# Performance work log

Measured on AMD Instinct MI355X. Metric: run time of the kernel, lower is better.

## Reference

```python
import jax, jax.numpy as jnp
import numpy as np

B, S, D, H, L, K = 16, 384, 512, 8, 4, 7
HD = D // H
MAXLEN = 400


def _pos_encoding(d=D, max_len=MAXLEN):
    # Faithful to the (unusual) torch loop: even idx i -> sin(pos/10000**(2i/d)),
    # odd idx i+1 -> cos(pos/10000**(2(i+1)/d))
    pe = np.zeros((max_len, d), dtype=np.float32)
    pos = np.arange(max_len, dtype=np.float64)[:, None]
    i = np.arange(0, d, 2)
    pe[:, i] = np.sin(pos / 10000.0 ** (2 * i / d))
    pe[:, i + 1] = np.cos(pos / 10000.0 ** (2 * (i + 1) / d))
    return jnp.asarray(pe)

POS_ENC = _pos_encoding()


def layer_norm(x, g, b, eps=1e-5):
    m = jnp.mean(x, -1, keepdims=True)
    v = jnp.mean((x - m) ** 2, -1, keepdims=True)
    return (x - m) * jax.lax.rsqrt(v + eps) * g + b


def dsconv(x, dw_w, pw_w, pw_b):
    # x: [B,S,D]; depthwise conv1d (no bias) then pointwise 1x1 (bias)
    xc = jnp.transpose(x, (0, 2, 1))  # [B,D,S]
    y = jax.lax.conv_general_dilated(
        xc, dw_w, window_strides=(1,), padding=[(K // 2, K // 2)],
        dimension_numbers=("NCH", "OIH", "NCH"), feature_group_count=D)  # [B,D,S]
    return jnp.einsum("bcs,oc->bso", y, pw_w) + pw_b  # [B,S,D]


def setup_inputs():
    key = jax.random.key(0)
    ks = jax.random.split(key, 16)
    sc = 0.02
    inp = {
        "x": jax.random.normal(ks[0], (B, S, D), jnp.float32),
        "mask": jax.random.randint(ks[1], (B, S), 0, 2, jnp.int32),
        "dw_w": jax.random.normal(ks[2], (L, D, 1, K), jnp.float32) * sc,
        "pw_w": jax.random.normal(ks[3], (L, D, D), jnp.float32) * sc,
        "pw_b": jnp.zeros((L, D), jnp.float32),
        "conv_ln_g": jnp.ones((L, D), jnp.float32),
        "conv_ln_b": jnp.zeros((L, D), jnp.float32),
        "pos_ln_g": jnp.ones((D,), jnp.float32),
        "pos_ln_b": jnp.zeros((D,), jnp.float32),
        "wq": jax.random.normal(ks[4], (D, D), jnp.float32) * sc,
        "bq": jnp.zeros((D,), jnp.float32),
        "wk": jax.random.normal(ks[5], (D, D), jnp.float32) * sc,
        "bk": jnp.zeros((D,), jnp.float32),
        "wv": jax.random.normal(ks[6], (D, D), jnp.float32) * sc,
        "bv": jnp.zeros((D,), jnp.float32),
        "wo": jax.random.normal(ks[7], (D, D), jnp.float32) * sc,
        "bo": jnp.zeros((D,), jnp.float32),
        "ff_ln_g": jnp.ones((D,), jnp.float32),
        "ff_ln_b": jnp.zeros((D,), jnp.float32),
        "ff_w": jax.random.normal(ks[8], (D, D), jnp.float32) * sc,
        "ff_b": jnp.zeros((D,), jnp.float32),
    }
    return inp


def attention(x, mask, wq, bq, wk, bk, wv, bv, wo, bo):
    def heads(w, b):
        y = jnp.einsum("bsd,od->bso", x, w) + b
        return jnp.transpose(y.reshape(B, S, H, HD), (0, 2, 1, 3))  # [B,H,S,HD]
    q, k, v = heads(wq, bq), heads(wk, bk), heads(wv, bv)
    energy = jnp.einsum("bhqd,bhkd->bhqk", q, k) / jnp.sqrt(jnp.float32(HD))
    m = (mask == 1)[:, None, None, :]  # [B,1,1,S]
    energy = jnp.where(m, jnp.float32(-1e10), energy)
    alpha = jax.nn.softmax(energy, axis=-1)  # dropout = identity (eval)
    a = jnp.einsum("bhqk,bhkd->bhqd", alpha, v)
    a = jnp.transpose(a, (0, 2, 1, 3)).reshape(B, S, D)
    return jnp.einsum("bsd,od->bso", a, wo) + bo


def reference(x, mask, dw_w, pw_w, pw_b, conv_ln_g, conv_ln_b, pos_ln_g, pos_ln_b,
              wq, bq, wk, bk, wv, bv, wo, bo, ff_ln_g, ff_ln_b, ff_w, ff_b):
    out = x + POS_ENC[None, :S, :]
    res = out
    out = layer_norm(out, pos_ln_g, pos_ln_b)
    for i in range(L):
        out = jax.nn.relu(dsconv(out, dw_w[i], pw_w[i], pw_b[i]))
        out = out + res  # dropout = identity (eval)
        res = out
        out = layer_norm(out, conv_ln_g[i], conv_ln_b[i])
    out = attention(out, mask, wq, bq, wk, bk, wv, bv, wo, bo)
    out = out + res
    res = out
    out = layer_norm(out, ff_ln_g, ff_ln_b)
    out = jax.nn.relu(jnp.einsum("bsd,od->bso", out, ff_w) + ff_b)
    return out + res
```

## Files before the change

kernel.cpp:

```cpp
#include <hip/hip_runtime.h>

#define BB 16
#define SS 384
#define DD 512
#define HH 8
#define HDIM 64
#define LLAY 4
#define KW 7
#define MM (BB*SS)

typedef unsigned short u16;
typedef unsigned int u32;
typedef short short8v __attribute__((ext_vector_type(8)));
typedef float floatx4 __attribute__((ext_vector_type(4)));

__device__ __forceinline__ float bf2f(u16 u) {
    union { u32 i; float f; } v; v.i = ((u32)u) << 16; return v.f;
}
__device__ __forceinline__ u16 f2bf(float f) {
    union { float f; u32 i; } v; v.f = f;
    return (u16)((v.i + 0x7FFFu + ((v.i >> 16) & 1u)) >> 16);
}
__device__ __forceinline__ bool sniff_f32(const void* dtp) {
    return *((const u32*)dtp) == 0x3F800000u;
}
__device__ __forceinline__ float ldf(const void* p, long i, bool f32) {
    return f32 ? ((const float*)p)[i] : bf2f(((const u16*)p)[i]);
}
__device__ __forceinline__ short8v ldfrag_scalar(const void* p, long i, bool f32) {
    short8v r;
    if (f32) {
        const float* q = (const float*)p + i;
#pragma unroll
        for (int j = 0; j < 8; j++) r[j] = (short)f2bf(q[j]);
    } else {
        r = *(const short8v*)((const u16*)p + i);
    }
    return r;
}

__device__ __forceinline__ void load_lds16(const u16* g, u16* l) {
    __builtin_amdgcn_global_load_lds((const __attribute__((address_space(1))) void*)g,
                                     (__attribute__((address_space(3))) void*)l, 16, 0, 0);
}
__device__ __forceinline__ int swz(int row) { return (row & 3) ^ ((row >> 2) & 3); }
__device__ __forceinline__ short8v lds_frag(const u16* buf, int row, int quad) {
    return *(const short8v*)(buf + ((size_t)row * 4 + (quad ^ swz(row))) * 8);
}

__device__ __forceinline__ floatx4 mfma16(short8v a, short8v b, floatx4 c) {
    return __builtin_amdgcn_mfma_f32_16x16x32_bf16(a, b, c, 0, 0, 0);
}

#define WCV_DW 2359296
#define WCV_TOT (WCV_DW + LLAY*KW*DD)
#define NCVB ((WCV_TOT + 255) / 256)

__global__ __launch_bounds__(256) void posln_cvt_kernel(
    const void* __restrict__ x, const void* __restrict__ g, const void* __restrict__ bvec,
    u16* __restrict__ res, u16* __restrict__ out,
    const void* __restrict__ pw_w, const void* __restrict__ wq,
    const void* __restrict__ wk, const void* __restrict__ wv,
    const void* __restrict__ wo, const void* __restrict__ ff_w,
    const void* __restrict__ dw_w, u16* __restrict__ wdst,
    const void* __restrict__ dtp) {
    const bool f32 = sniff_f32(dtp);
    const int tid = threadIdx.x;
    if (blockIdx.x >= MM) {
        const int i = (blockIdx.x - MM) * 256 + tid;
        if (i >= WCV_TOT) return;
        const void* src; long idx;
        if (i < 1048576) { src = pw_w; idx = i; }
        else if (i < WCV_DW) {
            const int j = i - 1048576;
            const int m = j >> 18;
            idx = j & 262143;
            src = (m == 0) ? wq : (m == 1) ? wk : (m == 2) ? wv : (m == 3) ? wo : ff_w;
        } else {
            const int j = i - WCV_DW;
            const int l = j / (KW * DD);
            const int r1 = j % (KW * DD);
            const int t = r1 / DD, c = r1 % DD;
            src = dw_w; idx = ((long)l * DD + c) * KW + t;
        }
        wdst[i] = f2bf(ldf(src, idx, f32));
        return;
    }
    const int row = blockIdx.x;
    const int s = row % SS;
    float v[2];
#pragma unroll
    for (int i = 0; i < 2; i++) {
        const int d = tid + i * 256;
        const float freq = __expf(-(float)d * 0.035977892078032f);
        const float arg = (float)s * freq;
        const float pe = (d & 1) ? __cosf(arg) : __sinf(arg);
        v[i] = ldf(x, (long)row * DD + d, f32) + pe;
        res[row * DD + d] = f2bf(v[i]);
    }
    float sum = v[0] + v[1], sq = v[0] * v[0] + v[1] * v[1];
#pragma unroll
    for (int off = 32; off; off >>= 1) { sum += __shfl_down(sum, off); sq += __shfl_down(sq, off); }
    __shared__ float red[4][2];
    const int wv2 = tid >> 6;
    if ((tid & 63) == 0) { red[wv2][0] = sum; red[wv2][1] = sq; }
    __syncthreads();
    sum = red[0][0] + red[1][0] + red[2][0] + red[3][0];
    sq  = red[0][1] + red[1][1] + red[2][1] + red[3][1];
    const float mean = sum * (1.f / DD);
    const float rstd = rsqrtf(sq * (1.f / DD) - mean * mean + 1e-5f);
#pragma unroll
    for (int i = 0; i < 2; i++) {
        const int d = tid + i * 256;
        out[row * DD + d] = f2bf((v[i] - mean) * rstd * ldf(g, d, f32) + ldf(bvec, d, f32));
    }
}

__global__ __launch_bounds__(512) void lnres_kernel(const u16* __restrict__ y,
                                                    const void* __restrict__ g,
                                                    const void* __restrict__ bvec,
                                                    int blayer,
                                                    u16* __restrict__ out,
                                                    const void* __restrict__ dtp) {
    const bool f32 = sniff_f32(dtp);
    const long voff = (long)blayer * DD;
    const int row = blockIdx.x * 8 + (threadIdx.x >> 6);
    const int lane = threadIdx.x & 63;
    const short8v v = *(const short8v*)(y + (size_t)row * DD + lane * 8);
    float f[8], sum = 0.f, sq = 0.f;
#pragma unroll
    for (int j = 0; j < 8; j++) { f[j] = bf2f((u16)v[j]); sum += f[j]; sq += f[j] * f[j]; }
#pragma unroll
    for (int off = 32; off; off >>= 1) { sum += __shfl_xor(sum, off); sq += __shfl_xor(sq, off); }
    const float mean = sum * (1.f / DD);
    const float rstd = rsqrtf(sq * (1.f / DD) - mean * mean + 1e-5f);
    short8v o;
#pragma unroll
    for (int j = 0; j < 8; j++) {
        const int d = lane * 8 + j;
        o[j] = (short)f2bf((f[j] - mean) * rstd * ldf(g, voff + d, f32) + ldf(bvec, voff + d, f32));
    }
    *(short8v*)(out + (size_t)row * DD + lane * 8) = o;
}

template <int VEC>
__global__ __launch_bounds__(256) void dwconv_kernel(const u16* __restrict__ in,
                                                     const void* __restrict__ w, int layer,
                                                     u16* __restrict__ out,
                                                     const void* __restrict__ dtp) {
    if constexpr (VEC) {
        const int bsw = (blockIdx.x & 7) * (MM * DD / 8 / 256 / 8) + (blockIdx.x >> 3);
        const int idx = bsw * 256 + threadIdx.x;
        const int c8 = (idx & 63) * 8;
        const int ms = idx >> 6;
        const int s = ms % SS;
        const u16* wl = (const u16*)w + (size_t)layer * KW * DD;
        float acc[8] = {0, 0, 0, 0, 0, 0, 0, 0};
#pragma unroll
        for (int t = 0; t < KW; t++) {
            const int ss2 = s + t - 3;
            if (ss2 >= 0 && ss2 < SS) {
                const short8v iv = *(const short8v*)(in + (size_t)(ms + t - 3) * DD + c8);
                const short8v wv = *(const short8v*)(wl + t * DD + c8);
#pragma unroll
                for (int j = 0; j < 8; j++)
                    acc[j] += bf2f((u16)iv[j]) * bf2f((u16)wv[j]);
            }
        }
        short8v ov;
#pragma unroll
        for (int j = 0; j < 8; j++) ov[j] = (short)f2bf(acc[j]);
        *(short8v*)(out + (size_t)ms * DD + c8) = ov;
    } else {
        const bool f32 = sniff_f32(dtp);
        const long woff = (long)layer * DD * KW;
        const int idx = blockIdx.x * 256 + threadIdx.x;
        const int c = idx & (DD - 1);
        const int ms = idx >> 9;
        const int s = ms % SS;
        float acc = 0.f;
#pragma unroll
        for (int t = 0; t < KW; t++) {
            const int ss2 = s + t - 3;
            if (ss2 >= 0 && ss2 < SS)
                acc += bf2f(in[(ms + t - 3) * DD + c]) * ldf(w, woff + c * KW + t, f32);
        }
        out[idx] = f2bf(acc);
    }
}

__device__ __forceinline__ void stage32(const u16* A, const u16* Wp, int m0,
                                        u16* Ab, u16* Wb, int tid, int k0) {
#pragma unroll
    for (int j = 0; j < 2; j++) {
        const int c = j * 256 + tid;
        const int row = c >> 2;
        const int kp = (c & 3) ^ swz(row);
        load_lds16(Wp + (size_t)row * DD + k0 + kp * 8, Wb + (size_t)c * 8);
    }
    if (tid < 128) {
        const int row = tid >> 2;
        const int kp = (tid & 3) ^ swz(row);
        load_lds16(A + (size_t)(m0 + row) * DD + k0 + kp * 8, Ab + (size_t)tid * 8);
    }
}

__device__ __forceinline__ void kloop32(const u16* A, const u16* Wp, int m0,
                                        u16* Abuf, u16* Wbuf,
                                        int tid, int wave, int ln15, int quad,
                                        floatx4 acc[2][2]) {
    stage32(A, Wp, m0, Abuf, Wbuf, tid, 0);
    __syncthreads();
    for (int ks = 0; ks < 16; ks++) {
        const int cur = ks & 1;
        u16* Ab = Abuf + cur * (32 * 32);
        u16* Wb = Wbuf + cur * (128 * 32);
        if (ks < 15)
            stage32(A, Wp, m0, Abuf + (cur ^ 1) * (32 * 32),
                    Wbuf + (cur ^ 1) * (128 * 32), tid, (ks + 1) * 32);
        const short8v a0 = lds_frag(Ab, ln15, quad);
        const short8v a1 = lds_frag(Ab, 16 + ln15, quad);
#pragma unroll
        for (int nt = 0; nt < 2; nt++) {
            const short8v b = lds_frag(Wb, wave * 32 + nt * 16 + ln15, quad);
            acc[0][nt] = mfma16(a0, b, acc[0][nt]);
            acc[1][nt] = mfma16(a1, b, acc[1][nt]);
        }
        __syncthreads();
    }
}

template <int RELU, int FINAL>
__global__ __launch_bounds__(256) void gemm32w_kernel(
    const u16* __restrict__ A, const u16* __restrict__ W,
    const void* __restrict__ bias, int blayer,
    const u16* __restrict__ res_in, u16* __restrict__ res_out,
    void* __restrict__ out, const void* __restrict__ dtp) {
    const bool f32 = sniff_f32(dtp);
    const long voff = (long)blayer * DD;
    __shared__ __align__(16) u16 smem[10240];
    u16* Wbuf = smem;
    u16* Abuf = smem + 8192;
    const int tid = threadIdx.x;
    const int m0 = blockIdx.x * 32, n0 = blockIdx.y * 128;
    const int wave = tid >> 6, lane = tid & 63;
    const int ln15 = lane & 15, quad = lane >> 4;

    floatx4 acc[2][2];
#pragma unroll
    for (int mt = 0; mt < 2; mt++)
#pragma unroll
        for (int nt = 0; nt < 2; nt++) acc[mt][nt] = {0.f, 0.f, 0.f, 0.f};

    kloop32(A, W + (size_t)n0 * DD, m0, Abuf, Wbuf, tid, wave, ln15, quad, acc);

#pragma unroll
    for (int nt = 0; nt < 2; nt++) {
        const int col = n0 + wave * 32 + nt * 16 + ln15;
        const float bval = ldf(bias, voff + col, f32);
#pragma unroll
        for (int mt = 0; mt < 2; mt++)
#pragma unroll
            for (int r = 0; r < 4; r++) {
                const int m = m0 + mt * 16 + quad * 4 + r;
                float y = acc[mt][nt][r] + bval;
                if (RELU) y = fmaxf(y, 0.f);
                y += bf2f(res_in[(size_t)m * DD + col]);
                if (res_out) res_out[(size_t)m * DD + col] = f2bf(y);
                if constexpr (FINAL) {
                    if (f32) ((float*)out)[(size_t)m * DD + col] = y;
                    else     ((u16*)out)[(size_t)m * DD + col] = f2bf(y);
                }
            }
    }
}

__device__ __forceinline__ void stage64(const u16* A, const u16* Wp, int m0,
                                        u16* Ab, u16* Wb, int tid, int k0) {
#pragma unroll
    for (int j = 0; j < 2; j++) {
        const int c = j * 256 + tid;
        const int row = c >> 2;
        const int kp = (c & 3) ^ swz(row);
        load_lds16(Wp + (size_t)row * DD + k0 + kp * 8, Wb + (size_t)c * 8);
    }
    {
        const int row = tid >> 2;
        const int kp = (tid & 3) ^ swz(row);
        load_lds16(A + (size_t)(m0 + row) * DD + k0 + kp * 8, Ab + (size_t)tid * 8);
    }
}

__device__ __forceinline__ void kloop64(const u16* A, const u16* Wp, int m0,
                                        u16* Abuf, u16* Wbuf,
                                        int tid, int wm, int wn, int ln15, int quad,
                                        floatx4 acc[2][4]) {
    stage64(A, Wp, m0, Abuf, Wbuf, tid, 0);
    __syncthreads();
    for (int ks = 0; ks < 16; ks++) {
        const int cur = ks & 1;
        u16* Ab = Abuf + cur * (64 * 32);
        u16* Wb = Wbuf + cur * (128 * 32);
        if (ks < 15)
            stage64(A, Wp, m0, Abuf + (cur ^ 1) * (64 * 32),
                    Wbuf + (cur ^ 1) * (128 * 32), tid, (ks + 1) * 32);
        const short8v a0 = lds_frag(Ab, wm * 32 + ln15, quad);
        const short8v a1 = lds_frag(Ab, wm * 32 + 16 + ln15, quad);
#pragma unroll
        for (int nt = 0; nt < 4; nt++) {
            const short8v b = lds_frag(Wb, wn * 64 + nt * 16 + ln15, quad);
            acc[0][nt] = mfma16(a0, b, acc[0][nt]);
            acc[1][nt] = mfma16(a1, b, acc[1][nt]);
        }
        __syncthreads();
    }
}

#define VP 72
__global__ __launch_bounds__(256, 4) void qkv64_kernel(
    const u16* __restrict__ A,
    const u16* __restrict__ Wq, const u16* __restrict__ Wk, const u16* __restrict__ Wv,
    const void* __restrict__ bq, const void* __restrict__ bk, const void* __restrict__ bv,
    u16* __restrict__ qo, u16* __restrict__ ko, u16* __restrict__ vo,
    const void* __restrict__ dtp) {
    const bool f32 = sniff_f32(dtp);
    const int sel = blockIdx.z;
    const u16* W = (sel == 0) ? Wq : (sel == 1) ? Wk : Wv;
    const void* bias = (sel == 0) ? bq : (sel == 1) ? bk : bv;

    __shared__ __align__(16) u16 smem[12288];
    u16* Wbuf = smem;
    u16* Abuf = smem + 8192;
    u16 (*vtile)[VP] = (u16 (*)[VP])smem;

    const int tid = threadIdx.x;
    const int m0 = blockIdx.x * 64, n0 = blockIdx.y * 128;
    const int wave = tid >> 6, lane = tid & 63;
    const int wm = wave >> 1, wn = wave & 1;
    const int ln15 = lane & 15, quad = lane >> 4;
    const int bidx = m0 / SS;

    floatx4 acc[2][4];
#pragma unroll
    for (int mt = 0; mt < 2; mt++)
#pragma unroll
        for (int nt = 0; nt < 4; nt++) acc[mt][nt] = {0.f, 0.f, 0.f, 0.f};

    kloop64(A, W + (size_t)n0 * DD, m0, Abuf, Wbuf, tid, wm, wn, ln15, quad, acc);

    if (sel == 2) {
#pragma unroll
        for (int nt = 0; nt < 4; nt++) {
            const int cl = wn * 64 + nt * 16 + ln15;
            const float bval = ldf(bias, n0 + cl, f32);
#pragma unroll
            for (int mt = 0; mt < 2; mt++)
#pragma unroll
                for (int r = 0; r < 4; r++)
                    vtile[cl][wm * 32 + mt * 16 + quad * 4 + r] = f2bf(acc[mt][nt][r] + bval);
        }
        __syncthreads();
        const int c = tid & 127, half = tid >> 7;
        const int col = n0 + c;
        const int h = col >> 6, hd = col & 63;
        u16* dst = vo + ((size_t)(bidx * HH + h) * HDIM + hd) * SS
                      + (m0 - bidx * SS) + half * 32;
        const u16* srcl = &vtile[c][half * 32];
#pragma unroll
        for (int j = 0; j < 4; j++)
            *(short8v*)(dst + j * 8) = *(const short8v*)(srcl + j * 8);
    } else {
        u16* out = (sel == 0) ? qo : ko;
#pragma unroll
        for (int nt = 0; nt < 4; nt++) {
            const int col = n0 + wn * 64 + nt * 16 + ln15;
            const int h = col >> 6, hd = col & 63;
            const float bval = ldf(bias, col, f32);
#pragma unroll
            for (int mt = 0; mt < 2; mt++)
#pragma unroll
                for (int r = 0; r < 4; r++) {
                    const int m = m0 + wm * 32 + mt * 16 + quad * 4 + r;
                    const int s = m - bidx * SS;
                    out[((size_t)(bidx * HH + h) * SS + s) * HDIM + hd] = f2bf(acc[mt][nt][r] + bval);
                }
        }
    }
}

template <int RELU, int DO_LN, int FINAL>
__global__ __launch_bounds__(512, 4) void gemm16_kernel(
    const u16* __restrict__ A, const void* __restrict__ W, int wlayer,
    const void* __restrict__ bias, const void* __restrict__ g,
    const void* __restrict__ bvec, int blayer,
    const u16* __restrict__ res_in, u16* __restrict__ res_out,
    void* __restrict__ out, const void* __restrict__ dtp) {
    const bool f32 = sniff_f32(dtp);
    const long woff = (long)wlayer * DD * DD;
    const long voff = (long)blayer * DD;
    __shared__ float part[8][16][2];
    const int tid = threadIdx.x;
    const int m0 = blockIdx.x * 16;
    const int wave = tid >> 6, lane = tid & 63;
    const int ln15 = lane & 15, quad = lane >> 4;

    floatx4 acc[4];
#pragma unroll
    for (int nt = 0; nt < 4; nt++) acc[nt] = {0.f, 0.f, 0.f, 0.f};

    const u16* A0 = A + (size_t)(m0 + ln15) * DD + quad * 8;
#pragma unroll
    for (int ks = 0; ks < 16; ks++) {
        const int k0 = ks * 32;
        short8v a0 = *(const short8v*)(A0 + k0);
        short8v b[4];
#pragma unroll
        for (int nt = 0; nt < 4; nt++) {
            const long wrow = woff + (long)(wave * 64 + nt * 16 + ln15) * DD + quad * 8 + k0;
            b[nt] = ldfrag_scalar(W, wrow, f32);
        }
#pragma unroll
        for (int nt = 0; nt < 4; nt++)
            acc[nt] = mfma16(a0, b[nt], acc[nt]);
    }

#pragma unroll
    for (int nt = 0; nt < 4; nt++) {
        const int col = wave * 64 + nt * 16 + ln15;
        const float bval = ldf(bias, voff + col, f32);
#pragma unroll
        for (int r = 0; r < 4; r++) {
            const int m = m0 + quad * 4 + r;
            float y = acc[nt][r] + bval;
            if (RELU) y = fmaxf(y, 0.f);
            y += bf2f(res_in[(size_t)m * DD + col]);
            if (res_out) res_out[(size_t)m * DD + col] = f2bf(y);
            acc[nt][r] = y;
        }
    }
    if constexpr (DO_LN) {
        float ls[4], lq[4];
#pragma unroll
        for (int r = 0; r < 4; r++) {
            float s = 0.f, q = 0.f;
#pragma unroll
            for (int nt = 0; nt < 4; nt++) { const float y = acc[nt][r]; s += y; q += y * y; }
            ls[r] = s; lq[r] = q;
        }
#pragma unroll
        for (int off = 1; off < 16; off <<= 1)
#pragma unroll
            for (int r = 0; r < 4; r++) {
                ls[r] += __shfl_xor(ls[r], off);
                lq[r] += __shfl_xor(lq[r], off);
            }
        if (ln15 == 0) {
#pragma unroll
            for (int r = 0; r < 4; r++) {
                part[wave][quad * 4 + r][0] = ls[r];
                part[wave][quad * 4 + r][1] = lq[r];
            }
        }
        __syncthreads();
        float mean[4], rstd[4];
#pragma unroll
        for (int r = 0; r < 4; r++) {
            const int rr = quad * 4 + r;
            float s = 0.f, q = 0.f;
#pragma unroll
            for (int wv = 0; wv < 8; wv++) { s += part[wv][rr][0]; q += part[wv][rr][1]; }
            const float mn = s * (1.f / DD);
            mean[r] = mn;
            rstd[r] = rsqrtf(q * (1.f / DD) - mn * mn + 1e-5f);
        }
#pragma unroll
        for (int nt = 0; nt < 4; nt++) {
            const int col = wave * 64 + nt * 16 + ln15;
            const float gv = ldf(g, voff + col, f32);
            const float bv = ldf(bvec, voff + col, f32);
#pragma unroll
            for (int r = 0; r < 4; r++) {
                const int m = m0 + quad * 4 + r;
                ((u16*)out)[(size_t)m * DD + col] =
                    f2bf((acc[nt][r] - mean[r]) * rstd[r] * gv + bv);
            }
        }
    } else {
#pragma unroll
        for (int nt = 0; nt < 4; nt++) {
            const int col = wave * 64 + nt * 16 + ln15;
#pragma unroll
            for (int r = 0; r < 4; r++) {
                const int m = m0 + quad * 4 + r;
                if (FINAL && f32) ((float*)out)[(size_t)m * DD + col] = acc[nt][r];
                else              ((u16*)out)[(size_t)m * DD + col] = f2bf(acc[nt][r]);
            }
        }
    }
}

__global__ __launch_bounds__(512, 4) void qkv16_kernel(
    const u16* __restrict__ A,
    const void* __restrict__ Wq, const void* __restrict__ Wk, const void* __restrict__ Wv,
    const void* __restrict__ bq, const void* __restrict__ bk, const void* __restrict__ bv,
    u16* __restrict__ qo, u16* __restrict__ ko, u16* __restrict__ vo,
    const void* __restrict__ dtp) {
    const bool f32 = sniff_f32(dtp);
    const int sel = blockIdx.y;
    const void* W = (sel == 0) ? Wq : (sel == 1) ? Wk : Wv;
    const void* bias = (sel == 0) ? bq : (sel == 1) ? bk : bv;

    const int tid = threadIdx.x;
    const int m0 = blockIdx.x * 16;
    const int wave = tid >> 6, lane = tid & 63;
    const int ln15 = lane & 15, quad = lane >> 4;
    const int bidx = m0 / SS;

    floatx4 acc[4];
#pragma unroll
    for (int nt = 0; nt < 4; nt++) acc[nt] = {0.f, 0.f, 0.f, 0.f};

    const u16* A0 = A + (size_t)(m0 + ln15) * DD + quad * 8;
#pragma unroll
    for (int ks = 0; ks < 16; ks++) {
        const int k0 = ks * 32;
        short8v a0 = *(const short8v*)(A0 + k0);
        short8v b[4];
#pragma unroll
        for (int nt = 0; nt < 4; nt++) {
            const long wrow = (long)(wave * 64 + nt * 16 + ln15) * DD + quad * 8 + k0;
            b[nt] = ldfrag_scalar(W, wrow, f32);
        }
#pragma unroll
        for (int nt = 0; nt < 4; nt++)
            acc[nt] = mfma16(a0, b[nt], acc[nt]);
    }

    if (sel == 2) {
#pragma unroll
        for (int nt = 0; nt < 4; nt++) {
            const int col = wave * 64 + nt * 16 + ln15;
            const int h = col >> 6, hd = col & 63;
            const float bval = ldf(bias, col, f32);
#pragma unroll
            for (int r = 0; r < 4; r++) {
                const int m = m0 + quad * 4 + r;
                const int s = m - bidx * SS;
                vo[((size_t)(bidx * HH + h) * HDIM + hd) * SS + s] = f2bf(acc[nt][r] + bval);
            }
        }
    } else {
        u16* out = (sel == 0) ? qo : ko;
#pragma unroll
        for (int nt = 0; nt < 4; nt++) {
            const int col = wave * 64 + nt * 16 + ln15;
            const int h = col >> 6, hd = col & 63;
            const float bval = ldf(bias, col, f32);
#pragma unroll
            for (int r = 0; r < 4; r++) {
                const int m = m0 + quad * 4 + r;
                const int s = m - bidx * SS;
                out[((size_t)(bidx * HH + h) * SS + s) * HDIM + hd] = f2bf(acc[nt][r] + bval);
            }
        }
    }
}

#define ALP 392
__global__ __launch_bounds__(256) void attn_kernel(const u16* __restrict__ q,
                                                   const u16* __restrict__ k,
                                                   const u16* __restrict__ vT,
                                                   const int* __restrict__ mask,
                                                   u16* __restrict__ out) {
    __shared__ __align__(16) u16 al4[4][16][ALP];

    const int n = blockIdx.x;
    const int i = n >> 3;
    const int g = (n & 7) * 16 + i / 6;
    const int sub = i % 6;
    const int h = g & 7, b = g >> 3;
    const int wave = threadIdx.x >> 6, lane = threadIdx.x & 63;
    const int ln15 = lane & 15, quad = lane >> 4;
    const int q0 = (sub * 4 + wave) * 16;

    const u16* qh = q + (size_t)(b * HH + h) * SS * HDIM;
    const u16* kh = k + (size_t)(b * HH + h) * SS * HDIM;

    const short8v* arow = (const short8v*)(qh + (q0 + ln15) * HDIM + quad * 8);
    const short8v a0 = arow[0], a1 = arow[4];

    floatx4 sc[24];
#pragma unroll
    for (int t = 0; t < 24; t++) {
        const short8v* brow = (const short8v*)(kh + (t * 16 + ln15) * HDIM + quad * 8);
        floatx4 acc = {0.f, 0.f, 0.f, 0.f};
        acc = mfma16(a0, brow[0], acc);
        acc = mfma16(a1, brow[4], acc);
        sc[t] = acc;
    }
    float mx[4] = {-3.0e38f, -3.0e38f, -3.0e38f, -3.0e38f};
#pragma unroll
    for (int t = 0; t < 24; t++) {
        const bool msk = (mask[b * SS + t * 16 + ln15] == 1);
#pragma unroll
        for (int r = 0; r < 4; r++) {
            float v = sc[t][r] * 0.125f;
            if (msk) v = -1e10f;
            sc[t][r] = v;
            mx[r] = fmaxf(mx[r], v);
        }
    }
#pragma unroll
    for (int off = 8; off; off >>= 1)
#pragma unroll
        for (int r = 0; r < 4; r++) mx[r] = fmaxf(mx[r], __shfl_xor(mx[r], off, 16));
    float sum[4] = {0.f, 0.f, 0.f, 0.f};
    u16* alw = &al4[wave][0][0];
#pragma unroll
    for (int t = 0; t < 24; t++) {
#pragma unroll
        for (int r = 0; r < 4; r++) {
            const float p = __expf(sc[t][r] - mx[r]);
            sum[r] += p;
            alw[(quad * 4 + r) * ALP + t * 16 + ln15] = f2bf(p);
        }
    }
#pragma unroll
    for (int off = 8; off; off >>= 1)
#pragma unroll
        for (int r = 0; r < 4; r++) sum[r] += __shfl_xor(sum[r], off, 16);
    __builtin_amdgcn_s_waitcnt(0);

    const u16* vh = vT + (size_t)(b * HH + h) * HDIM * SS;
#pragma unroll
    for (int dt = 0; dt < 4; dt++) {
        const int d0 = dt * 16;
        floatx4 acc = {0.f, 0.f, 0.f, 0.f};
#pragma unroll
        for (int k0 = 0; k0 < SS; k0 += 32) {
            const short8v af = *(const short8v*)(alw + ln15 * ALP + k0 + quad * 8);
            const short8v bf = *(const short8v*)(vh + (d0 + ln15) * SS + k0 + quad * 8);
            acc = mfma16(af, bf, acc);
        }
#pragma unroll
        for (int rr = 0; rr < 4; rr++) {
            const int s = q0 + quad * 4 + rr;
            out[((size_t)(b * SS + s)) * DD + h * HDIM + d0 + ln15] = f2bf(acc[rr] / sum[rr]);
        }
    }
}

extern "C" void kernel_launch(void* const* d_in, const int* in_sizes, int n_in,
                              void* d_out, int out_size, void* d_ws, size_t ws_size,
                              hipStream_t stream) {
    (void)in_sizes; (void)n_in; (void)out_size;
    const void* x     = d_in[0];
    const int*  mask  = (const int*)d_in[1];
    const void* dw_w  = d_in[2];
    const void* pw_w  = d_in[3];
    const void* pw_b  = d_in[4];
    const void* cln_g = d_in[5];
    const void* cln_b = d_in[6];
    const void* pln_g = d_in[7];
    const void* pln_b = d_in[8];
    const void* wq    = d_in[9];
    const void* bq    = d_in[10];
    const void* wk    = d_in[11];
    const void* bk    = d_in[12];
    const void* wv    = d_in[13];
    const void* bv    = d_in[14];
    const void* wo    = d_in[15];
    const void* bo    = d_in[16];
    const void* fln_g = d_in[17];
    const void* fln_b = d_in[18];
    const void* ff_w  = d_in[19];
    const void* ff_b  = d_in[20];
    const void* dtp   = cln_g;

    const size_t nAct = (size_t)MM * DD;
    char* p = (char*)d_ws;
    u16* res   = (u16*)p; p += nAct * 2;
    u16* lnout = (u16*)p; p += nAct * 2;
    u16* tmp   = (u16*)p; p += nAct * 2;
    u16* vT    = (u16*)p; p += nAct * 2;
    u16* wcv   = (u16*)p;
    u16* kb    = (u16*)d_out;

    const size_t needFast = nAct * 2 * 4 + (size_t)WCV_TOT * 2;
    const bool fast = (ws_size >= needFast);

    if (fast) {
        posln_cvt_kernel<<<MM + NCVB, 256, 0, stream>>>(
            x, pln_g, pln_b, res, lnout,
            pw_w, wq, wk, wv, wo, ff_w, dw_w, wcv, dtp);
        const u16* w_pw = wcv;
        const u16* w_q  = wcv + 1048576;
        const u16* w_k  = wcv + 1310720;
        const u16* w_v  = wcv + 1572864;
        const u16* w_o  = wcv + 1835008;
        const u16* w_ff = wcv + 2097152;
        const u16* w_dw = wcv + WCV_DW;

        for (int i = 0; i < LLAY; i++) {
            dwconv_kernel<1><<<MM * DD / 8 / 256, 256, 0, stream>>>(lnout, w_dw, i, tmp, dtp);
            gemm32w_kernel<1, 0><<<dim3(MM / 32, 4), 256, 0, stream>>>(
                tmp, w_pw + (size_t)i * DD * DD, pw_b, i, res, res, nullptr, dtp);
            lnres_kernel<<<MM / 8, 512, 0, stream>>>(res, cln_g, cln_b, i, lnout, dtp);
        }
        qkv64_kernel<<<dim3(MM / 64, 4, 3), 256, 0, stream>>>(
            lnout, w_q, w_k, w_v, bq, bk, bv, tmp, kb, vT, dtp);

        attn_kernel<<<BB * HH * (SS / 64), 256, 0, stream>>>(tmp, kb, vT, mask, lnout);

        gemm32w_kernel<0, 0><<<dim3(MM / 32, 4), 256, 0, stream>>>(
            lnout, w_o, bo, 0, res, res, nullptr, dtp);
        lnres_kernel<<<MM / 8, 512, 0, stream>>>(res, fln_g, fln_b, 0, lnout, dtp);
        gemm32w_kernel<1, 1><<<dim3(MM / 32, 4), 256, 0, stream>>>(
            lnout, w_ff, ff_b, 0, res, nullptr, d_out, dtp);
    } else {
        posln_cvt_kernel<<<MM, 256, 0, stream>>>(
            x, pln_g, pln_b, res, lnout,
            pw_w, wq, wk, wv, wo, ff_w, dw_w, (u16*)d_ws, dtp);
        for (int i = 0; i < LLAY; i++) {
            dwconv_kernel<0><<<MM * DD / 256, 256, 0, stream>>>(lnout, dw_w, i, tmp, dtp);
            gemm16_kernel<1, 1, 0><<<MM / 16, 512, 0, stream>>>(
                tmp, pw_w, i, pw_b, cln_g, cln_b, i, res, res, lnout, dtp);
        }
        qkv16_kernel<<<dim3(MM / 16, 3), 512, 0, stream>>>(
            lnout, wq, wk, wv, bq, bk, bv, tmp, kb, vT, dtp);

        attn_kernel<<<BB * HH * (SS / 64), 256, 0, stream>>>(tmp, kb, vT, mask, lnout);

        gemm16_kernel<0, 1, 0><<<MM / 16, 512, 0, stream>>>(
            lnout, wo, 0, bo, fln_g, fln_b, 0, res, res, lnout, dtp);
        gemm16_kernel<1, 0, 1><<<MM / 16, 512, 0, stream>>>(
            lnout, ff_w, 0, ff_b, nullptr, nullptr, 0, res, nullptr, d_out, dtp);
    }
}
```

Baseline: 359.1 us.

## Use 64-row GEMM tiles and stage K/V in LDS for attention

Replaces the 32x128 pointwise/output/FF GEMM with a 64x128 tile kernel that reuses the existing kloop64 (2x2 wave layout), halving the grid and improving weight reuse per block. Attention now cooperatively loads the whole per-head K and V^T into swizzled LDS before computing scores and the AV product, instead of each wave reading them directly from global memory. This raises LDS usage per attention block (about 96KB plus alpha buffers), which may cut occupancy, and the larger GEMM tiles reduce the number of blocks available to fill the device.

```diff
diff --git a/kernel.cpp b/kernel.cpp
--- a/kernel.cpp
+++ b/kernel.cpp
@@ -189,92 +189,6 @@
     }
 }
 
-__device__ __forceinline__ void stage32(const u16* A, const u16* Wp, int m0,
-                                        u16* Ab, u16* Wb, int tid, int k0) {
-#pragma unroll
-    for (int j = 0; j < 2; j++) {
-        const int c = j * 256 + tid;
-        const int row = c >> 2;
-        const int kp = (c & 3) ^ swz(row);
-        load_lds16(Wp + (size_t)row * DD + k0 + kp * 8, Wb + (size_t)c * 8);
-    }
-    if (tid < 128) {
-        const int row = tid >> 2;
-        const int kp = (tid & 3) ^ swz(row);
-        load_lds16(A + (size_t)(m0 + row) * DD + k0 + kp * 8, Ab + (size_t)tid * 8);
-    }
-}
-
-__device__ __forceinline__ void kloop32(const u16* A, const u16* Wp, int m0,
-                                        u16* Abuf, u16* Wbuf,
-                                        int tid, int wave, int ln15, int quad,
-                                        floatx4 acc[2][2]) {
-    stage32(A, Wp, m0, Abuf, Wbuf, tid, 0);
-    __syncthreads();
-    for (int ks = 0; ks < 16; ks++) {
-        const int cur = ks & 1;
-        u16* Ab = Abuf + cur * (32 * 32);
-        u16* Wb = Wbuf + cur * (128 * 32);
-        if (ks < 15)
-            stage32(A, Wp, m0, Abuf + (cur ^ 1) * (32 * 32),
-                    Wbuf + (cur ^ 1) * (128 * 32), tid, (ks + 1) * 32);
-        const short8v a0 = lds_frag(Ab, ln15, quad);
-        const short8v a1 = lds_frag(Ab, 16 + ln15, quad);
-#pragma unroll
-        for (int nt = 0; nt < 2; nt++) {
-            const short8v b = lds_frag(Wb, wave * 32 + nt * 16 + ln15, quad);
-            acc[0][nt] = mfma16(a0, b, acc[0][nt]);
-            acc[1][nt] = mfma16(a1, b, acc[1][nt]);
-        }
-        __syncthreads();
-    }
-}
-
-template <int RELU, int FINAL>
-__global__ __launch_bounds__(256) void gemm32w_kernel(
-    const u16* __restrict__ A, const u16* __restrict__ W,
-    const void* __restrict__ bias, int blayer,
-    const u16* __restrict__ res_in, u16* __restrict__ res_out,
-    void* __restrict__ out, const void* __restrict__ dtp) {
-    const bool f32 = sniff_f32(dtp);
-    const long voff = (long)blayer * DD;
-    __shared__ __align__(16) u16 smem[10240];
-    u16* Wbuf = smem;
-    u16* Abuf = smem + 8192;
-    const int tid = threadIdx.x;
-    const int m0 = blockIdx.x * 32, n0 = blockIdx.y * 128;
-    const int wave = tid >> 6, lane = tid & 63;
-    const int ln15 = lane & 15, quad = lane >> 4;
-
-    floatx4 acc[2][2];
-#pragma unroll
-    for (int mt = 0; mt < 2; mt++)
-#pragma unroll
-        for (int nt = 0; nt < 2; nt++) acc[mt][nt] = {0.f, 0.f, 0.f, 0.f};
-
-    kloop32(A, W + (size_t)n0 * DD, m0, Abuf, Wbuf, tid, wave, ln15, quad, acc);
-
-#pragma unroll
-    for (int nt = 0; nt < 2; nt++) {
-        const int col = n0 + wave * 32 + nt * 16 + ln15;
-        const float bval = ldf(bias, voff + col, f32);
-#pragma unroll
-        for (int mt = 0; mt < 2; mt++)
-#pragma unroll
-            for (int r = 0; r < 4; r++) {
-                const int m = m0 + mt * 16 + quad * 4 + r;
-                float y = acc[mt][nt][r] + bval;
-                if (RELU) y = fmaxf(y, 0.f);
-                y += bf2f(res_in[(size_t)m * DD + col]);
-                if (res_out) res_out[(size_t)m * DD + col] = f2bf(y);
-                if constexpr (FINAL) {
-                    if (f32) ((float*)out)[(size_t)m * DD + col] = y;
-                    else     ((u16*)out)[(size_t)m * DD + col] = f2bf(y);
-                }
-            }
-    }
-}
-
 __device__ __forceinline__ void stage64(const u16* A, const u16* Wp, int m0,
                                         u16* Ab, u16* Wb, int tid, int k0) {
 #pragma unroll
@@ -316,6 +230,52 @@
     }
 }
 
+template <int RELU, int FINAL>
+__global__ __launch_bounds__(256, 4) void gemm64_kernel(
+    const u16* __restrict__ A, const u16* __restrict__ W,
+    const void* __restrict__ bias, int blayer,
+    const u16* __restrict__ res_in, u16* __restrict__ res_out,
+    void* __restrict__ out, const void* __restrict__ dtp) {
+    const bool f32 = sniff_f32(dtp);
+    const long voff = (long)blayer * DD;
+    __shared__ __align__(16) u16 smem[12288];
+    u16* Wbuf = smem;
+    u16* Abuf = smem + 8192;
+    const int tid = threadIdx.x;
+    const int m0 = blockIdx.x * 64, n0 = blockIdx.y * 128;
+    const int wave = tid >> 6, lane = tid & 63;
+    const int wm = wave >> 1, wn = wave & 1;
+    const int ln15 = lane & 15, quad = lane >> 4;
+
+    floatx4 acc[2][4];
+#pragma unroll
+    for (int mt = 0; mt < 2; mt++)
+#pragma unroll
+        for (int nt = 0; nt < 4; nt++) acc[mt][nt] = {0.f, 0.f, 0.f, 0.f};
+
+    kloop64(A, W + (size_t)n0 * DD, m0, Abuf, Wbuf, tid, wm, wn, ln15, quad, acc);
+
+#pragma unroll
+    for (int nt = 0; nt < 4; nt++) {
+        const int col = n0 + wn * 64 + nt * 16 + ln15;
+        const float bval = ldf(bias, voff + col, f32);
+#pragma unroll
+        for (int mt = 0; mt < 2; mt++)
+#pragma unroll
+            for (int r = 0; r < 4; r++) {
+                const int m = m0 + wm * 32 + mt * 16 + quad * 4 + r;
+                float y = acc[mt][nt][r] + bval;
+                if (RELU) y = fmaxf(y, 0.f);
+                y += bf2f(res_in[(size_t)m * DD + col]);
+                if (res_out) res_out[(size_t)m * DD + col] = f2bf(y);
+                if constexpr (FINAL) {
+                    if (f32) ((float*)out)[(size_t)m * DD + col] = y;
+                    else     ((u16*)out)[(size_t)m * DD + col] = f2bf(y);
+                }
+            }
+    }
+}
+
 #define VP 72
 __global__ __launch_bounds__(256, 4) void qkv64_kernel(
     const u16* __restrict__ A,
@@ -572,6 +532,8 @@
                                                    const u16* __restrict__ vT,
                                                    const int* __restrict__ mask,
                                                    u16* __restrict__ out) {
+    __shared__ __align__(16) u16 Kb[3072 * 8];
+    __shared__ __align__(16) u16 Vb[3072 * 8];
     __shared__ __align__(16) u16 al4[4][16][ALP];
 
     const int n = blockIdx.x;
@@ -579,23 +541,43 @@
     const int g = (n & 7) * 16 + i / 6;
     const int sub = i % 6;
     const int h = g & 7, b = g >> 3;
-    const int wave = threadIdx.x >> 6, lane = threadIdx.x & 63;
+    const int tid = threadIdx.x;
+    const int wave = tid >> 6, lane = tid & 63;
     const int ln15 = lane & 15, quad = lane >> 4;
     const int q0 = (sub * 4 + wave) * 16;
 
     const u16* qh = q + (size_t)(b * HH + h) * SS * HDIM;
     const u16* kh = k + (size_t)(b * HH + h) * SS * HDIM;
-
+    const u16* vh = vT + (size_t)(b * HH + h) * HDIM * SS;
+
+#pragma unroll
+    for (int j = 0; j < 12; j++) {
+        const int c = j * 256 + tid;
+        const int row = c >> 3, cc = c & 7;
+        const int kp = cc ^ ((row ^ (row >> 3)) & 7);
+        load_lds16(kh + (size_t)row * HDIM + kp * 8, Kb + (size_t)c * 8);
+    }
+#pragma unroll
+    for (int j = 0; j < 12; j++) {
+        const int c = j * 256 + tid;
+        const int tile = c >> 8, rr = (c >> 2) & 63, cc = c & 3;
+        const int kp = cc ^ swz(rr);
+        load_lds16(vh + (size_t)rr * SS + tile * 32 + kp * 8, Vb + (size_t)c * 8);
+    }
     const short8v* arow = (const short8v*)(qh + (q0 + ln15) * HDIM + quad * 8);
     const short8v a0 = arow[0], a1 = arow[4];
+    __syncthreads();
 
     floatx4 sc[24];
 #pragma unroll
     for (int t = 0; t < 24; t++) {
-        const short8v* brow = (const short8v*)(kh + (t * 16 + ln15) * HDIM + quad * 8);
+        const int row = t * 16 + ln15;
+        const int s3 = (row ^ (row >> 3)) & 7;
+        const short8v b0 = *(const short8v*)(Kb + ((size_t)row * 8 + (quad ^ s3)) * 8);
+        const short8v b1 = *(const short8v*)(Kb + ((size_t)row * 8 + ((4 + quad) ^ s3)) * 8);
         floatx4 acc = {0.f, 0.f, 0.f, 0.f};
-        acc = mfma16(a0, brow[0], acc);
-        acc = mfma16(a1, brow[4], acc);
+        acc = mfma16(a0, b0, acc);
+        acc = mfma16(a1, b1, acc);
         sc[t] = acc;
     }
     float mx[4] = {-3.0e38f, -3.0e38f, -3.0e38f, -3.0e38f};
@@ -631,21 +613,21 @@
         for (int r = 0; r < 4; r++) sum[r] += __shfl_xor(sum[r], off, 16);
     __builtin_amdgcn_s_waitcnt(0);
 
-    const u16* vh = vT + (size_t)(b * HH + h) * HDIM * SS;
 #pragma unroll
     for (int dt = 0; dt < 4; dt++) {
-        const int d0 = dt * 16;
         floatx4 acc = {0.f, 0.f, 0.f, 0.f};
-#pragma unroll
-        for (int k0 = 0; k0 < SS; k0 += 32) {
-            const short8v af = *(const short8v*)(alw + ln15 * ALP + k0 + quad * 8);
-            const short8v bf = *(const short8v*)(vh + (d0 + ln15) * SS + k0 + quad * 8);
+        const int row = dt * 16 + ln15;
+        const int vsw = quad ^ swz(row);
+#pragma unroll
+        for (int c2 = 0; c2 < 12; c2++) {
+            const short8v af = *(const short8v*)(alw + ln15 * ALP + c2 * 32 + quad * 8);
+            const short8v bf = *(const short8v*)(Vb + ((size_t)c2 * 256 + row * 4 + vsw) * 8);
             acc = mfma16(af, bf, acc);
         }
 #pragma unroll
         for (int rr = 0; rr < 4; rr++) {
             const int s = q0 + quad * 4 + rr;
-            out[((size_t)(b * SS + s)) * DD + h * HDIM + d0 + ln15] = f2bf(acc[rr] / sum[rr]);
+            out[((size_t)(b * SS + s)) * DD + h * HDIM + dt * 16 + ln15] = f2bf(acc[rr] / sum[rr]);
         }
     }
 }
@@ -703,7 +685,7 @@
 
         for (int i = 0; i < LLAY; i++) {
             dwconv_kernel<1><<<MM * DD / 8 / 256, 256, 0, stream>>>(lnout, w_dw, i, tmp, dtp);
-            gemm32w_kernel<1, 0><<<dim3(MM / 32, 4), 256, 0, stream>>>(
+            gemm64_kernel<1, 0><<<dim3(MM / 64, 4), 256, 0, stream>>>(
                 tmp, w_pw + (size_t)i * DD * DD, pw_b, i, res, res, nullptr, dtp);
             lnres_kernel<<<MM / 8, 512, 0, stream>>>(res, cln_g, cln_b, i, lnout, dtp);
         }
@@ -712,10 +694,10 @@
 
         attn_kernel<<<BB * HH * (SS / 64), 256, 0, stream>>>(tmp, kb, vT, mask, lnout);
 
-        gemm32w_kernel<0, 0><<<dim3(MM / 32, 4), 256, 0, stream>>>(
+        gemm64_kernel<0, 0><<<dim3(MM / 64, 4), 256, 0, stream>>>(
             lnout, w_o, bo, 0, res, res, nullptr, dtp);
         lnres_kernel<<<MM / 8, 512, 0, stream>>>(res, fln_g, fln_b, 0, lnout, dtp);
-        gemm32w_kernel<1, 1><<<dim3(MM / 32, 4), 256, 0, stream>>>(
+        gemm64_kernel<1, 1><<<dim3(MM / 64, 4), 256, 0, stream>>>(
             lnout, w_ff, ff_b, 0, res, nullptr, d_out, dtp);
     } else {
         posln_cvt_kernel<<<MM, 256, 0, stream>>>(
```

Result: faster. 333.5 us (-7.1%).
